# Kernel optimization log

Measured on AMD Instinct MI355X. Metric: run time of the kernel, lower is better.

Reference implementation:

```python
import jax, jax.numpy as jnp
import numpy as np

N_BUILD = 200000
N_COMM = 10000
E_BUILD = 1200000
E_COMM = 160000
D_B = 64    # building feature dim
D_C = 32    # community feature dim
H = 64      # hidden dim (comm embedding)
D_FUSE = D_B + H  # 128
N_CLS = 2


def gcn(x, src, dst, W, b):
    """PyG-style GCNConv with self-loops and symmetric normalization.
    out_i = sum_{j->i} h_j / sqrt(deg_j * deg_i) + h_i / deg_i + b, h = x @ W.
    deg counts in-edges plus the self-loop."""
    n = x.shape[0]
    h = x @ W                                   # [n, out]
    deg = jnp.ones((n,), x.dtype).at[dst].add(1.0)
    norm = jax.lax.rsqrt(deg)
    msg = h[src] * (norm[src] * norm[dst])[:, None]          # gather + edge weight
    agg = jax.ops.segment_sum(msg, dst, num_segments=n)      # scatter-add
    return agg + h * (1.0 / deg)[:, None] + b


def setup_inputs():
    key = jax.random.key(0)
    ks = jax.random.split(key, 24)
    f32 = jnp.float32

    def glorot(k, shape):
        scale = np.sqrt(2.0 / (shape[0] + shape[1])).astype(np.float32)
        return jax.random.normal(k, shape, dtype=f32) * scale

    inp = {
        "building_features": jax.random.normal(ks[0], (N_BUILD, D_B), dtype=f32),
        "community_features": jax.random.normal(ks[1], (N_COMM, D_C), dtype=f32),
        # GCN weights: comm 32->64->64, attention 128->2, building 128->128->64->2
        "W_c1": glorot(ks[2], (D_C, H)),   "b_c1": jnp.zeros((H,), f32),
        "W_c2": glorot(ks[3], (H, H)),     "b_c2": jnp.zeros((H,), f32),
        "W_att": glorot(ks[4], (D_FUSE, 2)), "b_att": jnp.zeros((2,), f32),
        "W_b1": glorot(ks[5], (D_FUSE, D_FUSE)), "b_b1": jnp.zeros((D_FUSE,), f32),
        "W_b2": glorot(ks[6], (D_FUSE, H)),       "b_b2": jnp.zeros((H,), f32),
        "W_b3": glorot(ks[7], (H, N_CLS)),         "b_b3": jnp.zeros((N_CLS,), f32),
        # edge lists (int) and index maps
        "b_src": jax.random.randint(ks[8], (E_BUILD,), 0, N_BUILD, dtype=jnp.int32),
        "b_dst": jax.random.randint(ks[9], (E_BUILD,), 0, N_BUILD, dtype=jnp.int32),
        "c_src": jax.random.randint(ks[10], (E_COMM,), 0, N_COMM, dtype=jnp.int32),
        "c_dst": jax.random.randint(ks[11], (E_COMM,), 0, N_COMM, dtype=jnp.int32),
        "building_to_comm_mapping": jax.random.randint(ks[12], (N_BUILD,), 0, N_COMM, dtype=jnp.int32),
        # Batch.from_data_list ordering: here identity permutation of buildings
        "local_to_global": jnp.arange(N_BUILD, dtype=jnp.int32),
    }
    return inp


def reference(building_features, community_features,
              W_c1, b_c1, W_c2, b_c2, W_att, b_att,
              W_b1, b_b1, W_b2, b_b2, W_b3, b_b3,
              b_src, b_dst, c_src, c_dst,
              building_to_comm_mapping, local_to_global):
    # Community GNN (dropout is identity in eval)
    comm_x = jax.nn.relu(gcn(community_features, c_src, c_dst, W_c1, b_c1))
    comm_x = jax.nn.relu(gcn(comm_x, c_src, c_dst, W_c2, b_c2))

    # Irregular gather: per-building community embedding
    building_comm = comm_x[building_to_comm_mapping]          # [N_build, H]

    # Feature attention: softmax gate over the two modalities
    logits = jnp.concatenate([building_features, building_comm], axis=1) @ W_att + b_att
    a = jax.nn.softmax(logits, axis=1)                        # [N_build, 2]
    fused = jnp.concatenate([building_features * a[:, 0:1],
                             building_comm * a[:, 1:2]], axis=1)  # [N_build, 128]

    # Batched building GNN over disjoint per-community subgraphs
    local_x = fused[local_to_global]
    x = jax.nn.relu(gcn(local_x, b_src, b_dst, W_b1, b_b1))
    x = jax.nn.relu(gcn(x, b_src, b_dst, W_b2, b_b2))
    x = gcn(x, b_src, b_dst, W_b3, b_b3)                      # [N_build, 2]

    # Scatter back to global order, then log-softmax
    combined = jnp.zeros((building_features.shape[0], N_CLS), x.dtype)
    combined = combined.at[local_to_global].set(x)
    return jax.nn.log_softmax(combined, axis=1)
```

## Files before the change

kernel.cpp:

```cpp
#include <hip/hip_runtime.h>
#include <hip/hip_bf16.h>
#include <math.h>

#define N_BUILD 200000
#define N_COMM  10000
#define E_BUILD 1200000
#define E_COMM  160000
#define NB_B 196
#define NB_C 10

typedef __bf16 bf16x8 __attribute__((ext_vector_type(8)));
typedef float  f32x4  __attribute__((ext_vector_type(4)));

__device__ __forceinline__ unsigned short f2b(float f) {
    unsigned int u = __builtin_bit_cast(unsigned int, f);
    u += 0x7fffu + ((u >> 16) & 1u);
    return (unsigned short)(u >> 16);
}
__device__ __forceinline__ float b2f(unsigned short h) {
    unsigned int u = ((unsigned int)h) << 16;
    return __builtin_bit_cast(float, u);
}
__device__ __forceinline__ unsigned int pk2(float a, float b) {
    return (unsigned int)f2b(a) | ((unsigned int)f2b(b) << 16);
}
__device__ __forceinline__ void up8(uint4 v, float* r) {
    r[0] = b2f((unsigned short)v.x); r[1] = b2f((unsigned short)(v.x >> 16));
    r[2] = b2f((unsigned short)v.y); r[3] = b2f((unsigned short)(v.y >> 16));
    r[4] = b2f((unsigned short)v.z); r[5] = b2f((unsigned short)(v.z >> 16));
    r[6] = b2f((unsigned short)v.w); r[7] = b2f((unsigned short)(v.w >> 16));
}

#define INIT_TOT (N_BUILD + N_COMM + 2 * N_BUILD + N_COMM * 32 + 2048 + 4096 + 16384 + 8192)
__global__ __launch_bounds__(256) void init_k(int* cnt_b, int* cnt_c, float* out,
                                              const float* __restrict__ cF, unsigned short* __restrict__ cFb,
                                              const float* __restrict__ W_c1, unsigned short* __restrict__ Wt_c1,
                                              const float* __restrict__ W_c2, unsigned short* __restrict__ Wt_c2,
                                              const float* __restrict__ W_b1, unsigned short* __restrict__ Wt_b1,
                                              const float* __restrict__ W_b2, unsigned short* __restrict__ Wt_b2) {
    int i = blockIdx.x * blockDim.x + threadIdx.x;
    if (i < N_BUILD) { cnt_b[i] = 0; return; }
    i -= N_BUILD;
    if (i < N_COMM) { cnt_c[i] = 0; return; }
    i -= N_COMM;
    if (i < 2 * N_BUILD) { out[i] = -0.69314718056f; return; }
    i -= 2 * N_BUILD;
    if (i < N_COMM * 32) { cFb[i] = f2b(cF[i]); return; }
    i -= N_COMM * 32;
    if (i < 2048) { Wt_c1[(i % 64) * 32 + i / 64] = f2b(W_c1[i]); return; }
    i -= 2048;
    if (i < 4096) { Wt_c2[(i % 64) * 64 + i / 64] = f2b(W_c2[i]); return; }
    i -= 4096;
    if (i < 16384) { Wt_b1[(i % 128) * 128 + i / 128] = f2b(W_b1[i]); return; }
    i -= 16384;
    if (i < 8192) { Wt_b2[(i % 64) * 128 + i / 64] = f2b(W_b2[i]); }
}


__global__ __launch_bounds__(256) void hist2_k(int* cnt_b, const int* __restrict__ b_dst,
                                               int* cnt_c, const int* __restrict__ c_dst) {
    int i = blockIdx.x * blockDim.x + threadIdx.x;
    if (i < E_BUILD) atomicAdd(&cnt_b[b_dst[i]], 1);
    else if (i < E_BUILD + E_COMM) atomicAdd(&cnt_c[c_dst[i - E_BUILD]], 1);
}

__global__ __launch_bounds__(256) void scan1m_k(const int* __restrict__ cnt_b, int* __restrict__ ex_b, int* __restrict__ bs_b,
                                                const int* __restrict__ cnt_c, int* __restrict__ ex_c, int* __restrict__ bs_c) {
    __shared__ int sdata[256];
    const int tid = threadIdx.x;
    const int* cnt; int* ex; int* bs; int n, blk;
    if ((int)blockIdx.x < NB_B) { cnt = cnt_b; ex = ex_b; bs = bs_b; n = N_BUILD; blk = blockIdx.x; }
    else                        { cnt = cnt_c; ex = ex_c; bs = bs_c; n = N_COMM;  blk = blockIdx.x - NB_B; }
    const int base = blk * 1024 + tid * 4;
    int v[4]; int s = 0;
#pragma unroll
    for (int j = 0; j < 4; ++j) { v[j] = (base + j < n) ? cnt[base + j] : 0; s += v[j]; }
    sdata[tid] = s; __syncthreads();
    for (int off = 1; off < 256; off <<= 1) {
        int t = (tid >= off) ? sdata[tid - off] : 0;
        __syncthreads();
        sdata[tid] += t;
        __syncthreads();
    }
    if (tid == 255) bs[blk] = sdata[255];
    int run = sdata[tid] - s;
#pragma unroll
    for (int j = 0; j < 4; ++j) { if (base + j < n) ex[base + j] = run; run += v[j]; }
}

__global__ __launch_bounds__(256) void scan2m_k(int* bs_b, int* bs_c) {
    __shared__ int sdata[256];
    int* bs = (blockIdx.x == 0) ? bs_b : bs_c;
    int nb  = (blockIdx.x == 0) ? NB_B : NB_C;
    const int tid = threadIdx.x;
    int v = (tid < nb) ? bs[tid] : 0;
    sdata[tid] = v; __syncthreads();
    for (int off = 1; off < 256; off <<= 1) {
        int t = (tid >= off) ? sdata[tid - off] : 0;
        __syncthreads();
        sdata[tid] += t;
        __syncthreads();
    }
    if (tid < nb) bs[tid] = sdata[tid] - v;
}

__global__ __launch_bounds__(256) void finalizem_k(const int* __restrict__ cnt_b, int* rp_b, const int* __restrict__ bo_b,
                                                   int* cur_b, float* di_b,
                                                   const int* __restrict__ cnt_c, int* rp_c, const int* __restrict__ bo_c,
                                                   int* cur_c, float* di_c) {
    int i = blockIdx.x * blockDim.x + threadIdx.x;
    if (i < N_BUILD) {
        int cc = cnt_b[i];
        int r = rp_b[i] + bo_b[i >> 10];
        rp_b[i] = r; cur_b[i] = r; di_b[i] = 1.0f / (float)(cc + 1);
        if (i == 0) { rp_b[N_BUILD] = E_BUILD; rp_c[N_COMM] = E_COMM; }
    } else if (i < N_BUILD + N_COMM) {
        int ic = i - N_BUILD;
        int cc = cnt_c[ic];
        int r = rp_c[ic] + bo_c[ic >> 10];
        rp_c[ic] = r; cur_c[ic] = r; di_c[ic] = 1.0f / (float)(cc + 1);
    }
}

__global__ __launch_bounds__(256) void csr_scatterm_k(const int* __restrict__ b_src, const int* __restrict__ b_dst,
                                                      int* cur_b, const float* __restrict__ di_b, int2* __restrict__ cse_b,
                                                      const int* __restrict__ c_src, const int* __restrict__ c_dst,
                                                      int* cur_c, const float* __restrict__ di_c, int2* __restrict__ cse_c) {
    int i = blockIdx.x * blockDim.x + threadIdx.x;
    if (i < E_BUILD) {
        int s = b_src[i], d = b_dst[i];
        int pos = atomicAdd(&cur_b[d], 1);
        cse_b[pos] = make_int2(s, __float_as_int(sqrtf(di_b[s] * di_b[d])));
    } else if (i < E_BUILD + E_COMM) {
        int ie = i - E_BUILD;
        int s = c_src[ie], d = c_dst[ie];
        int pos = atomicAdd(&cur_c[d], 1);
        cse_c[pos] = make_int2(s, __float_as_int(sqrtf(di_c[s] * di_c[d])));
    }
}

template<int K, int N, bool GUARD>
__global__ __launch_bounds__(256) void gemm_mfma_k(const unsigned short* __restrict__ X,
                                                   const unsigned short* __restrict__ Wt,
                                                   unsigned short* __restrict__ H, int M) {
    constexpr int GPR = K / 8;
    __shared__ unsigned short sA[64 * K];
    __shared__ unsigned short sB[N * K];
    const int tid  = threadIdx.x;
    const int row0 = blockIdx.x * 64;

    for (int idx = tid; idx < 64 * GPR; idx += 256) {
        int r = idx / GPR, g = idx % GPR;
        uint4 v = make_uint4(0u, 0u, 0u, 0u);
        if (!GUARD || row0 + r < M)
            v = *(const uint4*)&X[(size_t)(row0 + r) * K + g * 8];
        int gs = g ^ (r & (GPR - 1));
        *(uint4*)&sA[r * K + gs * 8] = v;
    }
    for (int idx = tid; idx < N * GPR; idx += 256) {
        int r = idx / GPR, g = idx % GPR;
        uint4 v = *(const uint4*)&Wt[(size_t)r * K + g * 8];
        int gs = g ^ (r & (GPR - 1));
        *(uint4*)&sB[r * K + gs * 8] = v;
    }
    __syncthreads();

    const int wave = tid >> 6, lane = tid & 63;
    const int rA = wave * 16 + (lane & 15);
    const int kg = lane >> 4;

    f32x4 zero = {0.f, 0.f, 0.f, 0.f};
    f32x4 acc[N / 16];
#pragma unroll
    for (int t = 0; t < N / 16; ++t) acc[t] = zero;

#pragma unroll
    for (int ks = 0; ks < K / 32; ++ks) {
        int gA = (ks * 4 + kg) ^ (rA & (GPR - 1));
        bf16x8 a = *(const bf16x8*)&sA[rA * K + gA * 8];
#pragma unroll
        for (int t = 0; t < N / 16; ++t) {
            int rB = t * 16 + (lane & 15);
            int gB = (ks * 4 + kg) ^ (rB & (GPR - 1));
            bf16x8 b = *(const bf16x8*)&sB[rB * K + gB * 8];
            acc[t] = __builtin_amdgcn_mfma_f32_16x16x32_bf16(a, b, acc[t], 0, 0, 0);
        }
    }

    const int crow = wave * 16 + (lane >> 4) * 4;
    const int ccol = lane & 15;
#pragma unroll
    for (int t = 0; t < N / 16; ++t) {
#pragma unroll
        for (int j = 0; j < 4; ++j) {
            int r = row0 + crow + j;
            if (!GUARD || r < M)
                H[(size_t)r * N + t * 16 + ccol] = f2b(acc[t][j]);
        }
    }
}

__global__ __launch_bounds__(256) void gemm_att_k(const float* __restrict__ bF,
                                                  const unsigned short* __restrict__ cx,
                                                  const int* __restrict__ map,
                                                  const int* __restrict__ l2g,
                                                  const float* __restrict__ Watt,
                                                  const float* __restrict__ batt,
                                                  const unsigned short* __restrict__ Wt,
                                                  unsigned short* __restrict__ H) {
    constexpr int K = 128, N = 128, GPR = 16;
    __shared__ unsigned short sA[64 * K];
    __shared__ unsigned short sB[N * K];
    __shared__ float sWt[256];
    const int tid = threadIdx.x;
    const int row0 = blockIdx.x * 64;
    sWt[tid] = Watt[tid];
    for (int idx = tid; idx < N * GPR; idx += 256) {
        int r = idx / GPR, g = idx % GPR;
        uint4 v = *(const uint4*)&Wt[(size_t)r * K + g * 8];
        int gs = g ^ (r & (GPR - 1));
        *(uint4*)&sB[r * K + gs * 8] = v;
    }
    __syncthreads();
    {
        const int r = tid >> 2, j = tid & 3;
        const int g = l2g[row0 + r];
        float vals[32];
        if (j < 2) {
            const float* f1 = &bF[(size_t)g * 64 + j * 32];
#pragma unroll
            for (int t = 0; t < 8; ++t) {
                float4 v = *(const float4*)&f1[t * 4];
                vals[t*4+0]=v.x; vals[t*4+1]=v.y; vals[t*4+2]=v.z; vals[t*4+3]=v.w;
            }
        } else {
            const unsigned short* f2 = &cx[(size_t)map[g] * 64 + (j & 1) * 32];
#pragma unroll
            for (int t = 0; t < 4; ++t) {
                uint4 u = *(const uint4*)&f2[t * 8];
                up8(u, &vals[t * 8]);
            }
        }
        float l0 = 0.f, l1 = 0.f;
        const int ch0 = j * 32;
#pragma unroll
        for (int t = 0; t < 32; ++t) {
            l0 = fmaf(vals[t], sWt[(ch0 + t) * 2 + 0], l0);
            l1 = fmaf(vals[t], sWt[(ch0 + t) * 2 + 1], l1);
        }
        l0 += __shfl_xor(l0, 1, 4); l0 += __shfl_xor(l0, 2, 4);
        l1 += __shfl_xor(l1, 1, 4); l1 += __shfl_xor(l1, 2, 4);
        l0 += batt[0]; l1 += batt[1];
        float mm = fmaxf(l0, l1);
        float e0 = __expf(l0 - mm), e1 = __expf(l1 - mm);
        float a = ((j < 2) ? e0 : e1) / (e0 + e1);
#pragma unroll
        for (int t = 0; t < 4; ++t) {
            uint4 o;
            o.x = pk2(vals[t*8+0]*a, vals[t*8+1]*a);
            o.y = pk2(vals[t*8+2]*a, vals[t*8+3]*a);
            o.z = pk2(vals[t*8+4]*a, vals[t*8+5]*a);
            o.w = pk2(vals[t*8+6]*a, vals[t*8+7]*a);
            int gi = j * 4 + t;
            int gs = gi ^ (r & (GPR - 1));
            *(uint4*)&sA[r * K + gs * 8] = o;
        }
    }
    __syncthreads();
    const int wave = tid >> 6, lane = tid & 63;
    const int rA = wave * 16 + (lane & 15);
    const int kg = lane >> 4;
    f32x4 zero = {0.f, 0.f, 0.f, 0.f};
    f32x4 acc[8];
#pragma unroll
    for (int t = 0; t < 8; ++t) acc[t] = zero;
#pragma unroll
    for (int ks = 0; ks < 4; ++ks) {
        int gA = (ks * 4 + kg) ^ (rA & 15);
        bf16x8 a = *(const bf16x8*)&sA[rA * K + gA * 8];
#pragma unroll
        for (int t = 0; t < 8; ++t) {
            int rB = t * 16 + (lane & 15);
            int gB = (ks * 4 + kg) ^ (rB & 15);
            bf16x8 b = *(const bf16x8*)&sB[rB * K + gB * 8];
            acc[t] = __builtin_amdgcn_mfma_f32_16x16x32_bf16(a, b, acc[t], 0, 0, 0);
        }
    }
    const int crow = wave * 16 + (lane >> 4) * 4;
    const int ccol = lane & 15;
#pragma unroll
    for (int t = 0; t < 8; ++t)
#pragma unroll
        for (int jj = 0; jj < 4; ++jj)
            H[(size_t)(row0 + crow + jj) * N + t * 16 + ccol] = f2b(acc[t][jj]);
}

template<bool RELU>
__global__ __launch_bounds__(256) void gather128b_k(const int* __restrict__ rowptr,
                                                    const int2* __restrict__ cse,
                                                    const unsigned short* __restrict__ h,
                                                    const float* __restrict__ dinv,
                                                    const float* __restrict__ bias,
                                                    unsigned short* __restrict__ out, int nPair) {
    int wid = (blockIdx.x * blockDim.x + threadIdx.x) >> 6;
    int lane = threadIdx.x & 63;
    if (wid >= nPair) return;
    int node = wid * 2 + (lane >> 5);
    int sl = lane & 31, c = sl * 4;
    int beg = rowptr[node], end = rowptr[node + 1];
    uint2 hv = *(const uint2*)&h[(size_t)node * 128 + c];
    float iv = dinv[node];
    float4 bb = *(const float4*)&bias[c];
    float a0 = 0.f, a1 = 0.f, a2 = 0.f, a3 = 0.f;
    for (int p = beg; p < end; p += 8) {
        int2 q[8]; uint2 v[8];
#pragma unroll
        for (int t = 0; t < 8; ++t) { int e = p + t; q[t] = cse[e < end ? e : 0]; }
#pragma unroll
        for (int t = 0; t < 8; ++t) v[t] = *(const uint2*)&h[(size_t)q[t].x * 128 + c];
#pragma unroll
        for (int t = 0; t < 8; ++t) {
            float w = (p + t < end) ? __int_as_float(q[t].y) : 0.f;
            a0 = fmaf(b2f((unsigned short)v[t].x), w, a0);
            a1 = fmaf(b2f((unsigned short)(v[t].x >> 16)), w, a1);
            a2 = fmaf(b2f((unsigned short)v[t].y), w, a2);
            a3 = fmaf(b2f((unsigned short)(v[t].y >> 16)), w, a3);
        }
    }
    float o0 = fmaf(b2f((unsigned short)hv.x), iv, a0) + bb.x;
    float o1 = fmaf(b2f((unsigned short)(hv.x >> 16)), iv, a1) + bb.y;
    float o2 = fmaf(b2f((unsigned short)hv.y), iv, a2) + bb.z;
    float o3 = fmaf(b2f((unsigned short)(hv.y >> 16)), iv, a3) + bb.w;
    if (RELU) {
        o0 = fmaxf(o0, 0.f); o1 = fmaxf(o1, 0.f);
        o2 = fmaxf(o2, 0.f); o3 = fmaxf(o3, 0.f);
    }
    uint2 ov; ov.x = pk2(o0, o1); ov.y = pk2(o2, o3);
    *(uint2*)&out[(size_t)node * 128 + c] = ov;
}

template<bool RELU>
__global__ __launch_bounds__(256) void gather64x4_k(const int* __restrict__ rowptr,
                                                    const int2* __restrict__ cse,
                                                    const unsigned short* __restrict__ h,
                                                    const float* __restrict__ dinv,
                                                    const float* __restrict__ bias,
                                                    unsigned short* __restrict__ out, int nQuad) {
    int wid = (blockIdx.x * blockDim.x + threadIdx.x) >> 6;
    int lane = threadIdx.x & 63;
    if (wid >= nQuad) return;
    int node = wid * 4 + (lane >> 4);
    int sl = lane & 15, c = sl * 4;
    int beg = rowptr[node], end = rowptr[node + 1];
    uint2 hv = *(const uint2*)&h[(size_t)node * 64 + c];
    float iv = dinv[node];
    float4 bb = *(const float4*)&bias[c];
    float a0 = 0.f, a1 = 0.f, a2 = 0.f, a3 = 0.f;
    for (int p = beg; p < end; p += 8) {
        int2 q[8]; uint2 v[8];
#pragma unroll
        for (int t = 0; t < 8; ++t) { int e = p + t; q[t] = cse[e < end ? e : 0]; }
#pragma unroll
        for (int t = 0; t < 8; ++t) v[t] = *(const uint2*)&h[(size_t)q[t].x * 64 + c];
#pragma unroll
        for (int t = 0; t < 8; ++t) {
            float w = (p + t < end) ? __int_as_float(q[t].y) : 0.f;
            a0 = fmaf(b2f((unsigned short)v[t].x), w, a0);
            a1 = fmaf(b2f((unsigned short)(v[t].x >> 16)), w, a1);
            a2 = fmaf(b2f((unsigned short)v[t].y), w, a2);
            a3 = fmaf(b2f((unsigned short)(v[t].y >> 16)), w, a3);
        }
    }
    float o0 = fmaf(b2f((unsigned short)hv.x), iv, a0) + bb.x;
    float o1 = fmaf(b2f((unsigned short)(hv.x >> 16)), iv, a1) + bb.y;
    float o2 = fmaf(b2f((unsigned short)hv.y), iv, a2) + bb.z;
    float o3 = fmaf(b2f((unsigned short)(hv.y >> 16)), iv, a3) + bb.w;
    if (RELU) {
        o0 = fmaxf(o0, 0.f); o1 = fmaxf(o1, 0.f);
        o2 = fmaxf(o2, 0.f); o3 = fmaxf(o3, 0.f);
    }
    uint2 ov; ov.x = pk2(o0, o1); ov.y = pk2(o2, o3);
    *(uint2*)&out[(size_t)node * 64 + c] = ov;
}

__global__ __launch_bounds__(256) void gather64_dot_k(const int* __restrict__ rowptr,
                                                      const int2* __restrict__ cse,
                                                      const unsigned short* __restrict__ h,
                                                      const float* __restrict__ dinv,
                                                      const float* __restrict__ bias,
                                                      const float* __restrict__ W3,
                                                      float* __restrict__ Dh, int nQuad) {
    int wid = (blockIdx.x * blockDim.x + threadIdx.x) >> 6;
    int lane = threadIdx.x & 63;
    if (wid >= nQuad) return;
    int node = wid * 4 + (lane >> 4);
    int sl = lane & 15, c = sl * 4;
    int beg = rowptr[node], end = rowptr[node + 1];
    uint2 hv = *(const uint2*)&h[(size_t)node * 64 + c];
    float iv = dinv[node];
    float4 bb = *(const float4*)&bias[c];
    float4 w01 = *(const float4*)&W3[c * 2];
    float4 w23 = *(const float4*)&W3[c * 2 + 4];
    float a0 = 0.f, a1 = 0.f, a2 = 0.f, a3 = 0.f;
    for (int p = beg; p < end; p += 8) {
        int2 q[8]; uint2 v[8];
#pragma unroll
        for (int t = 0; t < 8; ++t) { int e = p + t; q[t] = cse[e < end ? e : 0]; }
#pragma unroll
        for (int t = 0; t < 8; ++t) v[t] = *(const uint2*)&h[(size_t)q[t].x * 64 + c];
#pragma unroll
        for (int t = 0; t < 8; ++t) {
            float w = (p + t < end) ? __int_as_float(q[t].y) : 0.f;
            a0 = fmaf(b2f((unsigned short)v[t].x), w, a0);
            a1 = fmaf(b2f((unsigned short)(v[t].x >> 16)), w, a1);
            a2 = fmaf(b2f((unsigned short)v[t].y), w, a2);
            a3 = fmaf(b2f((unsigned short)(v[t].y >> 16)), w, a3);
        }
    }
    float o0 = fmaxf(fmaf(b2f((unsigned short)hv.x), iv, a0) + bb.x, 0.f);
    float o1 = fmaxf(fmaf(b2f((unsigned short)(hv.x >> 16)), iv, a1) + bb.y, 0.f);
    float o2 = fmaxf(fmaf(b2f((unsigned short)hv.y), iv, a2) + bb.z, 0.f);
    float o3 = fmaxf(fmaf(b2f((unsigned short)(hv.y >> 16)), iv, a3) + bb.w, 0.f);
    float d0 = o0 * w01.x + o1 * w01.z + o2 * w23.x + o3 * w23.z;
    float d1 = o0 * w01.y + o1 * w01.w + o2 * w23.y + o3 * w23.w;
#pragma unroll
    for (int m = 1; m < 16; m <<= 1) {
        d0 += __shfl_xor(d0, m, 16);
        d1 += __shfl_xor(d1, m, 16);
    }
    if (sl == 0) {
        Dh[2 * (size_t)node + 0] = d0;
        Dh[2 * (size_t)node + 1] = d1;
    }
}

__global__ __launch_bounds__(256) void gather2_logsm_k(const int* __restrict__ rowptr,
                                                       const int2* __restrict__ cse,
                                                       const float* __restrict__ h2,
                                                       const float* __restrict__ dinv,
                                                       const float* __restrict__ bias,
                                                       const int* __restrict__ l2g,
                                                       float* __restrict__ out, int n) {
    int i = blockIdx.x * blockDim.x + threadIdx.x;
    if (i >= n) return;
    int beg = rowptr[i], end = rowptr[i + 1];
    float2 hv = *(const float2*)&h2[2 * (size_t)i];
    float iv = dinv[i];
    float a = 0.f, b = 0.f;
    for (int p = beg; p < end; p += 8) {
        int2 q[8]; float2 v[8];
#pragma unroll
        for (int t = 0; t < 8; ++t) { int e = p + t; q[t] = cse[e < end ? e : 0]; }
#pragma unroll
        for (int t = 0; t < 8; ++t) v[t] = *(const float2*)&h2[2 * (size_t)q[t].x];
#pragma unroll
        for (int t = 0; t < 8; ++t) {
            float w = (p + t < end) ? __int_as_float(q[t].y) : 0.f;
            a = fmaf(v[t].x, w, a);
            b = fmaf(v[t].y, w, b);
        }
    }
    a = fmaf(hv.x, iv, a) + bias[0];
    b = fmaf(hv.y, iv, b) + bias[1];
    float m = fmaxf(a, b);
    float ls = m + logf(__expf(a - m) + __expf(b - m));
    int g = l2g[i];
    out[2 * (size_t)g + 0] = a - ls;
    out[2 * (size_t)g + 1] = b - ls;
}


static inline dim3 g1(long long n, int tpb = 256) { return dim3((unsigned)((n + tpb - 1) / tpb)); }

extern "C" void kernel_launch(void* const* d_in, const int* in_sizes, int n_in,
                              void* d_out, int out_size, void* d_ws, size_t ws_size,
                              hipStream_t stream) {
    const float* bF   = (const float*)d_in[0];
    const float* cF   = (const float*)d_in[1];
    const float* W_c1 = (const float*)d_in[2];
    const float* b_c1 = (const float*)d_in[3];
    const float* W_c2 = (const float*)d_in[4];
    const float* b_c2 = (const float*)d_in[5];
    const float* W_at = (const float*)d_in[6];
    const float* b_at = (const float*)d_in[7];
    const float* W_b1 = (const float*)d_in[8];
    const float* b_b1 = (const float*)d_in[9];
    const float* W_b2 = (const float*)d_in[10];
    const float* b_b2 = (const float*)d_in[11];
    const float* W_b3 = (const float*)d_in[12];
    const float* b_b3 = (const float*)d_in[13];
    const int* b_src = (const int*)d_in[14];
    const int* b_dst = (const int*)d_in[15];
    const int* c_src = (const int*)d_in[16];
    const int* c_dst = (const int*)d_in[17];
    const int* map   = (const int*)d_in[18];
    const int* l2g   = (const int*)d_in[19];
    float* out = (float*)d_out;

    char* p = (char*)d_ws;
    auto alloc = [&](size_t bytes) { char* q = p; p += (bytes + 15) & ~(size_t)15; return q; };
    int*   cnt_b    = (int*)  alloc(N_BUILD * 4);
    int*   rowptr_b = (int*)  alloc((N_BUILD + 4) * 4);
    int*   cursor_b = (int*)  alloc(N_BUILD * 4);
    int*   bsum_b   = (int*)  alloc(256 * 4);
    int*   cnt_c    = (int*)  alloc(N_COMM * 4);
    int*   rowptr_c = (int*)  alloc((N_COMM + 4) * 4);
    int*   cursor_c = (int*)  alloc(N_COMM * 4);
    int*   bsum_c   = (int*)  alloc(256 * 4);
    int2*  cse_b    = (int2*) alloc((size_t)E_BUILD * 8);
    int2*  cse_c    = (int2*) alloc((size_t)E_COMM * 8);
    float* dinv_b   = (float*)alloc(N_BUILD * 4);
    float* dinv_c   = (float*)alloc(N_COMM * 4);
    unsigned short* cFb    = (unsigned short*)alloc((size_t)N_COMM * 32 * 2);
    unsigned short* Wt_c1  = (unsigned short*)alloc(64 * 32 * 2);
    unsigned short* Wt_c2  = (unsigned short*)alloc(64 * 64 * 2);
    unsigned short* Wt_b1  = (unsigned short*)alloc(128 * 128 * 2);
    unsigned short* Wt_b2  = (unsigned short*)alloc(64 * 128 * 2);
    unsigned short* ch_bf  = (unsigned short*)alloc((size_t)N_COMM * 64 * 2);
    unsigned short* cx1_bf = (unsigned short*)alloc((size_t)N_COMM * 64 * 2);
    unsigned short* cx2_bf = (unsigned short*)alloc((size_t)N_COMM * 64 * 2);
    unsigned short* A_bf   = (unsigned short*)alloc((size_t)N_BUILD * 128 * 2);
    unsigned short* B_bf   = (unsigned short*)alloc((size_t)N_BUILD * 128 * 2);
    float* Dh = (float*)alloc((size_t)N_BUILD * 2 * 4);

    init_k<<<g1(INIT_TOT), 256, 0, stream>>>(cnt_b, cnt_c, out,
                                             cF, cFb, W_c1, Wt_c1, W_c2, Wt_c2, W_b1, Wt_b1, W_b2, Wt_b2);
    hist2_k<<<g1(E_BUILD + E_COMM), 256, 0, stream>>>(cnt_b, b_dst, cnt_c, c_dst);
    scan1m_k<<<NB_B + NB_C, 256, 0, stream>>>(cnt_b, rowptr_b, bsum_b, cnt_c, rowptr_c, bsum_c);
    scan2m_k<<<2, 256, 0, stream>>>(bsum_b, bsum_c);
    finalizem_k<<<g1(N_BUILD + N_COMM), 256, 0, stream>>>(cnt_b, rowptr_b, bsum_b, cursor_b, dinv_b,
                                                          cnt_c, rowptr_c, bsum_c, cursor_c, dinv_c);
    csr_scatterm_k<<<g1(E_BUILD + E_COMM), 256, 0, stream>>>(b_src, b_dst, cursor_b, dinv_b, cse_b,
                                                             c_src, c_dst, cursor_c, dinv_c, cse_c);

    gemm_mfma_k<32, 64, true><<<dim3((N_COMM + 63) / 64), 256, 0, stream>>>(cFb, Wt_c1, ch_bf, N_COMM);
    gather64x4_k<true><<<g1((long long)(N_COMM / 4) * 64), 256, 0, stream>>>(rowptr_c, cse_c, ch_bf, dinv_c, b_c1, cx1_bf, N_COMM / 4);

    gemm_mfma_k<64, 64, true><<<dim3((N_COMM + 63) / 64), 256, 0, stream>>>(cx1_bf, Wt_c2, ch_bf, N_COMM);
    gather64x4_k<true><<<g1((long long)(N_COMM / 4) * 64), 256, 0, stream>>>(rowptr_c, cse_c, ch_bf, dinv_c, b_c2, cx2_bf, N_COMM / 4);

    gemm_att_k<<<dim3(N_BUILD / 64), 256, 0, stream>>>(bF, cx2_bf, map, l2g, W_at, b_at, Wt_b1, B_bf);
    gather128b_k<true><<<g1((long long)(N_BUILD / 2) * 64), 256, 0, stream>>>(rowptr_b, cse_b, B_bf, dinv_b, b_b1, A_bf, N_BUILD / 2);

    gemm_mfma_k<128, 64, false><<<dim3(N_BUILD / 64), 256, 0, stream>>>(A_bf, Wt_b2, B_bf, N_BUILD);
    gather64_dot_k<<<g1((long long)(N_BUILD / 4) * 64), 256, 0, stream>>>(rowptr_b, cse_b, B_bf, dinv_b, b_b2, W_b3, Dh, N_BUILD / 4);

    gather2_logsm_k<<<g1(N_BUILD), 256, 0, stream>>>(rowptr_b, cse_b, Dh, dinv_b, b_b3, l2g, out, N_BUILD);
}
```

Measured before the change: 358.7 us.

## Partition CSR scatter by destination range and widen gather loads to 16 bytes

The CSR scatter kernel now gives each 2048-edge chunk to 8 blocks. Each block handles only the destinations in one eighth of the node range, so concurrent atomics and cse writes land in a narrower address window, which should improve L2 locality. The cost is that every block reads the whole dst chunk, so dst is read 8 times. The gather kernels now use 8 bf16 per lane with uint4 loads, so fewer lanes serve each node and more nodes fit per wave. This doubles the vector width of the neighbour-row fetches but can leave more lanes idle when degrees vary.

```diff
diff --git a/kernel.cpp b/kernel.cpp
--- a/kernel.cpp
+++ b/kernel.cpp
@@ -8,6 +8,9 @@
 #define E_COMM  160000
 #define NB_B 196
 #define NB_C 10
+#define CHUNK 2048
+#define CB_B ((E_BUILD + CHUNK - 1) / CHUNK)
+#define CB_C ((E_COMM  + CHUNK - 1) / CHUNK)
 
 typedef __bf16 bf16x8 __attribute__((ext_vector_type(8)));
 typedef float  f32x4  __attribute__((ext_vector_type(4)));
@@ -122,20 +125,34 @@
     }
 }
 
-__global__ __launch_bounds__(256) void csr_scatterm_k(const int* __restrict__ b_src, const int* __restrict__ b_dst,
+template<int NDIV>
+__device__ __forceinline__ void scatter_part(const int* __restrict__ src, const int* __restrict__ dst,
+                                             int* cur, const float* __restrict__ di,
+                                             int2* __restrict__ cse, int E, int cid, int x) {
+    int base = cid * CHUNK + threadIdx.x;
+#pragma unroll
+    for (int j = 0; j < CHUNK / 256; ++j, base += 256) {
+        if (base < E) {
+            int d = dst[base];
+            if ((unsigned)d / (unsigned)NDIV == (unsigned)x) {
+                int s = src[base];
+                int pos = atomicAdd(&cur[d], 1);
+                cse[pos] = make_int2(s, __float_as_int(sqrtf(di[s] * di[d])));
+            }
+        }
+    }
+}
+
+__global__ __launch_bounds__(256) void csr_scatterp_k(const int* __restrict__ b_src, const int* __restrict__ b_dst,
                                                       int* cur_b, const float* __restrict__ di_b, int2* __restrict__ cse_b,
                                                       const int* __restrict__ c_src, const int* __restrict__ c_dst,
                                                       int* cur_c, const float* __restrict__ di_c, int2* __restrict__ cse_c) {
-    int i = blockIdx.x * blockDim.x + threadIdx.x;
-    if (i < E_BUILD) {
-        int s = b_src[i], d = b_dst[i];
-        int pos = atomicAdd(&cur_b[d], 1);
-        cse_b[pos] = make_int2(s, __float_as_int(sqrtf(di_b[s] * di_b[d])));
-    } else if (i < E_BUILD + E_COMM) {
-        int ie = i - E_BUILD;
-        int s = c_src[ie], d = c_dst[ie];
-        int pos = atomicAdd(&cur_c[d], 1);
-        cse_c[pos] = make_int2(s, __float_as_int(sqrtf(di_c[s] * di_c[d])));
+    int bid = blockIdx.x;
+    if (bid < 8 * CB_B) {
+        scatter_part<N_BUILD / 8>(b_src, b_dst, cur_b, di_b, cse_b, E_BUILD, bid >> 3, bid & 7);
+    } else {
+        bid -= 8 * CB_B;
+        scatter_part<N_COMM / 8>(c_src, c_dst, cur_c, di_c, cse_c, E_COMM, bid >> 3, bid & 7);
     }
 }
 
@@ -295,92 +312,56 @@
             H[(size_t)(row0 + crow + jj) * N + t * 16 + ccol] = f2b(acc[t][jj]);
 }
 
-template<bool RELU>
-__global__ __launch_bounds__(256) void gather128b_k(const int* __restrict__ rowptr,
-                                                    const int2* __restrict__ cse,
-                                                    const unsigned short* __restrict__ h,
-                                                    const float* __restrict__ dinv,
-                                                    const float* __restrict__ bias,
-                                                    unsigned short* __restrict__ out, int nPair) {
+template<int F, bool RELU>
+__global__ __launch_bounds__(256) void gatherF_k(const int* __restrict__ rowptr,
+                                                 const int2* __restrict__ cse,
+                                                 const unsigned short* __restrict__ h,
+                                                 const float* __restrict__ dinv,
+                                                 const float* __restrict__ bias,
+                                                 unsigned short* __restrict__ out, int nGrp) {
+    constexpr int LPN = F / 8;
+    constexpr int NPW = 64 / LPN;
     int wid = (blockIdx.x * blockDim.x + threadIdx.x) >> 6;
     int lane = threadIdx.x & 63;
-    if (wid >= nPair) return;
-    int node = wid * 2 + (lane >> 5);
-    int sl = lane & 31, c = sl * 4;
+    if (wid >= nGrp) return;
+    int node = wid * NPW + lane / LPN;
+    int c = (lane % LPN) * 8;
     int beg = rowptr[node], end = rowptr[node + 1];
-    uint2 hv = *(const uint2*)&h[(size_t)node * 128 + c];
+    uint4 hv = *(const uint4*)&h[(size_t)node * F + c];
     float iv = dinv[node];
-    float4 bb = *(const float4*)&bias[c];
-    float a0 = 0.f, a1 = 0.f, a2 = 0.f, a3 = 0.f;
+    float4 bb0 = *(const float4*)&bias[c];
+    float4 bb1 = *(const float4*)&bias[c + 4];
+    float acc[8];
+#pragma unroll
+    for (int i = 0; i < 8; ++i) acc[i] = 0.f;
     for (int p = beg; p < end; p += 8) {
-        int2 q[8]; uint2 v[8];
+        int2 q[8]; uint4 v[8];
 #pragma unroll
         for (int t = 0; t < 8; ++t) { int e = p + t; q[t] = cse[e < end ? e : 0]; }
 #pragma unroll
-        for (int t = 0; t < 8; ++t) v[t] = *(const uint2*)&h[(size_t)q[t].x * 128 + c];
+        for (int t = 0; t < 8; ++t) v[t] = *(const uint4*)&h[(size_t)q[t].x * F + c];
 #pragma unroll
         for (int t = 0; t < 8; ++t) {
             float w = (p + t < end) ? __int_as_float(q[t].y) : 0.f;
-            a0 = fmaf(b2f((unsigned short)v[t].x), w, a0);
-            a1 = fmaf(b2f((unsigned short)(v[t].x >> 16)), w, a1);
-            a2 = fmaf(b2f((unsigned short)v[t].y), w, a2);
-            a3 = fmaf(b2f((unsigned short)(v[t].y >> 16)), w, a3);
-        }
-    }
-    float o0 = fmaf(b2f((unsigned short)hv.x), iv, a0) + bb.x;
-    float o1 = fmaf(b2f((unsigned short)(hv.x >> 16)), iv, a1) + bb.y;
-    float o2 = fmaf(b2f((unsigned short)hv.y), iv, a2) + bb.z;
-    float o3 = fmaf(b2f((unsigned short)(hv.y >> 16)), iv, a3) + bb.w;
+            float r[8]; up8(v[t], r);
+#pragma unroll
+            for (int i = 0; i < 8; ++i) acc[i] = fmaf(r[i], w, acc[i]);
+        }
+    }
+    float hr[8]; up8(hv, hr);
+    float o[8];
+    o[0] = fmaf(hr[0], iv, acc[0]) + bb0.x; o[1] = fmaf(hr[1], iv, acc[1]) + bb0.y;
+    o[2] = fmaf(hr[2], iv, acc[2]) + bb0.z; o[3] = fmaf(hr[3], iv, acc[3]) + bb0.w;
+    o[4] = fmaf(hr[4], iv, acc[4]) + bb1.x; o[5] = fmaf(hr[5], iv, acc[5]) + bb1.y;
+    o[6] = fmaf(hr[6], iv, acc[6]) + bb1.z; o[7] = fmaf(hr[7], iv, acc[7]) + bb1.w;
     if (RELU) {
-        o0 = fmaxf(o0, 0.f); o1 = fmaxf(o1, 0.f);
-        o2 = fmaxf(o2, 0.f); o3 = fmaxf(o3, 0.f);
-    }
-    uint2 ov; ov.x = pk2(o0, o1); ov.y = pk2(o2, o3);
-    *(uint2*)&out[(size_t)node * 128 + c] = ov;
-}
-
-template<bool RELU>
-__global__ __launch_bounds__(256) void gather64x4_k(const int* __restrict__ rowptr,
-                                                    const int2* __restrict__ cse,
-                                                    const unsigned short* __restrict__ h,
-                                                    const float* __restrict__ dinv,
-                                                    const float* __restrict__ bias,
-                                                    unsigned short* __restrict__ out, int nQuad) {
-    int wid = (blockIdx.x * blockDim.x + threadIdx.x) >> 6;
-    int lane = threadIdx.x & 63;
-    if (wid >= nQuad) return;
-    int node = wid * 4 + (lane >> 4);
-    int sl = lane & 15, c = sl * 4;
-    int beg = rowptr[node], end = rowptr[node + 1];
-    uint2 hv = *(const uint2*)&h[(size_t)node * 64 + c];
-    float iv = dinv[node];
-    float4 bb = *(const float4*)&bias[c];
-    float a0 = 0.f, a1 = 0.f, a2 = 0.f, a3 = 0.f;
-    for (int p = beg; p < end; p += 8) {
-        int2 q[8]; uint2 v[8];
-#pragma unroll
-        for (int t = 0; t < 8; ++t) { int e = p + t; q[t] = cse[e < end ? e : 0]; }
-#pragma unroll
-        for (int t = 0; t < 8; ++t) v[t] = *(const uint2*)&h[(size_t)q[t].x * 64 + c];
-#pragma unroll
-        for (int t = 0; t < 8; ++t) {
-            float w = (p + t < end) ? __int_as_float(q[t].y) : 0.f;
-            a0 = fmaf(b2f((unsigned short)v[t].x), w, a0);
-            a1 = fmaf(b2f((unsigned short)(v[t].x >> 16)), w, a1);
-            a2 = fmaf(b2f((unsigned short)v[t].y), w, a2);
-            a3 = fmaf(b2f((unsigned short)(v[t].y >> 16)), w, a3);
-        }
-    }
-    float o0 = fmaf(b2f((unsigned short)hv.x), iv, a0) + bb.x;
-    float o1 = fmaf(b2f((unsigned short)(hv.x >> 16)), iv, a1) + bb.y;
-    float o2 = fmaf(b2f((unsigned short)hv.y), iv, a2) + bb.z;
-    float o3 = fmaf(b2f((unsigned short)(hv.y >> 16)), iv, a3) + bb.w;
-    if (RELU) {
-        o0 = fmaxf(o0, 0.f); o1 = fmaxf(o1, 0.f);
-        o2 = fmaxf(o2, 0.f); o3 = fmaxf(o3, 0.f);
-    }
-    uint2 ov; ov.x = pk2(o0, o1); ov.y = pk2(o2, o3);
-    *(uint2*)&out[(size_t)node * 64 + c] = ov;
+#pragma unroll
+        for (int i = 0; i < 8; ++i) o[i] = fmaxf(o[i], 0.f);
+    }
+    uint4 ov;
+    ov.x = pk2(o[0], o[1]); ov.y = pk2(o[2], o[3]);
+    ov.z = pk2(o[4], o[5]); ov.w = pk2(o[6], o[7]);
+    *(uint4*)&out[(size_t)node * F + c] = ov;
 }
 
 __global__ __launch_bounds__(256) void gather64_dot_k(const int* __restrict__ rowptr,
@@ -389,44 +370,55 @@
                                                       const float* __restrict__ dinv,
                                                       const float* __restrict__ bias,
                                                       const float* __restrict__ W3,
-                                                      float* __restrict__ Dh, int nQuad) {
+                                                      float* __restrict__ Dh, int nOct) {
     int wid = (blockIdx.x * blockDim.x + threadIdx.x) >> 6;
     int lane = threadIdx.x & 63;
-    if (wid >= nQuad) return;
-    int node = wid * 4 + (lane >> 4);
-    int sl = lane & 15, c = sl * 4;
+    if (wid >= nOct) return;
+    int node = wid * 8 + (lane >> 3);
+    int sl = lane & 7, c = sl * 8;
     int beg = rowptr[node], end = rowptr[node + 1];
-    uint2 hv = *(const uint2*)&h[(size_t)node * 64 + c];
+    uint4 hv = *(const uint4*)&h[(size_t)node * 64 + c];
     float iv = dinv[node];
-    float4 bb = *(const float4*)&bias[c];
-    float4 w01 = *(const float4*)&W3[c * 2];
-    float4 w23 = *(const float4*)&W3[c * 2 + 4];
-    float a0 = 0.f, a1 = 0.f, a2 = 0.f, a3 = 0.f;
+    float4 bb0 = *(const float4*)&bias[c];
+    float4 bb1 = *(const float4*)&bias[c + 4];
+    float4 w4[4];
+#pragma unroll
+    for (int i = 0; i < 4; ++i) w4[i] = *(const float4*)&W3[c * 2 + i * 4];
+    float acc[8];
+#pragma unroll
+    for (int i = 0; i < 8; ++i) acc[i] = 0.f;
     for (int p = beg; p < end; p += 8) {
-        int2 q[8]; uint2 v[8];
+        int2 q[8]; uint4 v[8];
 #pragma unroll
         for (int t = 0; t < 8; ++t) { int e = p + t; q[t] = cse[e < end ? e : 0]; }
 #pragma unroll
-        for (int t = 0; t < 8; ++t) v[t] = *(const uint2*)&h[(size_t)q[t].x * 64 + c];
+        for (int t = 0; t < 8; ++t) v[t] = *(const uint4*)&h[(size_t)q[t].x * 64 + c];
 #pragma unroll
         for (int t = 0; t < 8; ++t) {
             float w = (p + t < end) ? __int_as_float(q[t].y) : 0.f;
-            a0 = fmaf(b2f((unsigned short)v[t].x), w, a0);
-            a1 = fmaf(b2f((unsigned short)(v[t].x >> 16)), w, a1);
-            a2 = fmaf(b2f((unsigned short)v[t].y), w, a2);
-            a3 = fmaf(b2f((unsigned short)(v[t].y >> 16)), w, a3);
-        }
-    }
-    float o0 = fmaxf(fmaf(b2f((unsigned short)hv.x), iv, a0) + bb.x, 0.f);
-    float o1 = fmaxf(fmaf(b2f((unsigned short)(hv.x >> 16)), iv, a1) + bb.y, 0.f);
-    float o2 = fmaxf(fmaf(b2f((unsigned short)hv.y), iv, a2) + bb.z, 0.f);
-    float o3 = fmaxf(fmaf(b2f((unsigned short)(hv.y >> 16)), iv, a3) + bb.w, 0.f);
-    float d0 = o0 * w01.x + o1 * w01.z + o2 * w23.x + o3 * w23.z;
-    float d1 = o0 * w01.y + o1 * w01.w + o2 * w23.y + o3 * w23.w;
-#pragma unroll
-    for (int m = 1; m < 16; m <<= 1) {
-        d0 += __shfl_xor(d0, m, 16);
-        d1 += __shfl_xor(d1, m, 16);
+            float r[8]; up8(v[t], r);
+#pragma unroll
+            for (int i = 0; i < 8; ++i) acc[i] = fmaf(r[i], w, acc[i]);
+        }
+    }
+    float hr[8]; up8(hv, hr);
+    float o[8];
+    o[0] = fmaf(hr[0], iv, acc[0]) + bb0.x; o[1] = fmaf(hr[1], iv, acc[1]) + bb0.y;
+    o[2] = fmaf(hr[2], iv, acc[2]) + bb0.z; o[3] = fmaf(hr[3], iv, acc[3]) + bb0.w;
+    o[4] = fmaf(hr[4], iv, acc[4]) + bb1.x; o[5] = fmaf(hr[5], iv, acc[5]) + bb1.y;
+    o[6] = fmaf(hr[6], iv, acc[6]) + bb1.z; o[7] = fmaf(hr[7], iv, acc[7]) + bb1.w;
+#pragma unroll
+    for (int i = 0; i < 8; ++i) o[i] = fmaxf(o[i], 0.f);
+    float d0 = 0.f, d1 = 0.f;
+#pragma unroll
+    for (int i = 0; i < 4; ++i) {
+        d0 = fmaf(o[2*i],   w4[i].x, d0); d0 = fmaf(o[2*i+1], w4[i].z, d0);
+        d1 = fmaf(o[2*i],   w4[i].y, d1); d1 = fmaf(o[2*i+1], w4[i].w, d1);
+    }
+#pragma unroll
+    for (int m = 1; m < 8; m <<= 1) {
+        d0 += __shfl_xor(d0, m, 8);
+        d1 += __shfl_xor(d1, m, 8);
     }
     if (sl == 0) {
         Dh[2 * (size_t)node + 0] = d0;
@@ -530,20 +522,20 @@
     scan2m_k<<<2, 256, 0, stream>>>(bsum_b, bsum_c);
     finalizem_k<<<g1(N_BUILD + N_COMM), 256, 0, stream>>>(cnt_b, rowptr_b, bsum_b, cursor_b, dinv_b,
                                                           cnt_c, rowptr_c, bsum_c, cursor_c, dinv_c);
-    csr_scatterm_k<<<g1(E_BUILD + E_COMM), 256, 0, stream>>>(b_src, b_dst, cursor_b, dinv_b, cse_b,
-                                                             c_src, c_dst, cursor_c, dinv_c, cse_c);
+    csr_scatterp_k<<<8 * (CB_B + CB_C), 256, 0, stream>>>(b_src, b_dst, cursor_b, dinv_b, cse_b,
+                                                          c_src, c_dst, cursor_c, dinv_c, cse_c);
 
     gemm_mfma_k<32, 64, true><<<dim3((N_COMM + 63) / 64), 256, 0, stream>>>(cFb, Wt_c1, ch_bf, N_COMM);
-    gather64x4_k<true><<<g1((long long)(N_COMM / 4) * 64), 256, 0, stream>>>(rowptr_c, cse_c, ch_bf, dinv_c, b_c1, cx1_bf, N_COMM / 4);
+    gatherF_k<64, true><<<g1((long long)(N_COMM / 8) * 64), 256, 0, stream>>>(rowptr_c, cse_c, ch_bf, dinv_c, b_c1, cx1_bf, N_COMM / 8);
 
     gemm_mfma_k<64, 64, true><<<dim3((N_COMM + 63) / 64), 256, 0, stream>>>(cx1_bf, Wt_c2, ch_bf, N_COMM);
-    gather64x4_k<true><<<g1((long long)(N_COMM / 4) * 64), 256, 0, stream>>>(rowptr_c, cse_c, ch_bf, dinv_c, b_c2, cx2_bf, N_COMM / 4);
+    gatherF_k<64, true><<<g1((long long)(N_COMM / 8) * 64), 256, 0, stream>>>(rowptr_c, cse_c, ch_bf, dinv_c, b_c2, cx2_bf, N_COMM / 8);
 
     gemm_att_k<<<dim3(N_BUILD / 64), 256, 0, stream>>>(bF, cx2_bf, map, l2g, W_at, b_at, Wt_b1, B_bf);
-    gather128b_k<true><<<g1((long long)(N_BUILD / 2) * 64), 256, 0, stream>>>(rowptr_b, cse_b, B_bf, dinv_b, b_b1, A_bf, N_BUILD / 2);
+    gatherF_k<128, true><<<g1((long long)(N_BUILD / 4) * 64), 256, 0, stream>>>(rowptr_b, cse_b, B_bf, dinv_b, b_b1, A_bf, N_BUILD / 4);
 
     gemm_mfma_k<128, 64, false><<<dim3(N_BUILD / 64), 256, 0, stream>>>(A_bf, Wt_b2, B_bf, N_BUILD);
-    gather64_dot_k<<<g1((long long)(N_BUILD / 4) * 64), 256, 0, stream>>>(rowptr_b, cse_b, B_bf, dinv_b, b_b2, W_b3, Dh, N_BUILD / 4);
+    gather64_dot_k<<<g1((long long)(N_BUILD / 8) * 64), 256, 0, stream>>>(rowptr_b, cse_b, B_bf, dinv_b, b_b2, W_b3, Dh, N_BUILD / 8);
 
     gather2_logsm_k<<<g1(N_BUILD), 256, 0, stream>>>(rowptr_b, cse_b, Dh, dinv_b, b_b3, l2g, out, N_BUILD);
 }
```

Result: faster. 338.9 us (-5.5%).
